# Performance work log

Hardware: AMD Instinct MI355X
Metric: run time of the kernel (lower is better)

The kernel has to match this reference:

```python
import jax, jax.numpy as jnp
import numpy as np

N, T, D, H = 32, 1024, 512, 512


def setup_inputs() -> dict:
    key = jax.random.key(0)
    k1, k2, k3, k4 = jax.random.split(key, 4)
    x = jax.random.normal(k1, (N, T, D), dtype=jnp.float32)
    h0 = jax.random.normal(k2, (N, H), dtype=jnp.float32)
    Wx = jax.random.normal(k3, (D, 4 * H), dtype=jnp.float32) / np.sqrt(D)
    Wh = jax.random.normal(k4, (H, 4 * H), dtype=jnp.float32) / np.sqrt(H)
    b = jnp.zeros((4 * H,), dtype=jnp.float32)
    return {"x": x, "h0": h0, "Wx": Wx, "Wh": Wh, "b": b}


def reference(x, h0, Wx, Wh, b):
    Hdim = h0.shape[1]
    # Precompute input projection for all timesteps: (N,T,4H)
    xW = jnp.einsum('ntd,dk->ntk', x, Wx) + b

    def step(carry, xw_t):
        h, c = carry
        a = xw_t + h @ Wh  # (N,4H)
        i = jax.nn.sigmoid(a[:, :Hdim])
        f = jax.nn.sigmoid(a[:, Hdim:2 * Hdim])
        o = jax.nn.sigmoid(a[:, 2 * Hdim:3 * Hdim])
        g = jnp.tanh(a[:, 3 * Hdim:])
        c_next = f * c + i * g
        h_next = o * jnp.tanh(c_next)
        return (h_next, c_next), h_next

    c0 = jnp.zeros_like(h0)
    xW_t = jnp.swapaxes(xW, 0, 1)  # (T,N,4H) for scan over time
    _, hs = jax.lax.scan(step, (h0, c0), xW_t)
    return jnp.swapaxes(hs, 0, 1)  # (N,T,H)
```

## Files before the change

kernel.cpp:

```cpp
#include <hip/hip_runtime.h>
#include <hip/hip_bf16.h>


#define NWG 32
#define LDW 520
#define SMEM_BYTES (2*64*LDW*2 + 4*32*16*4 + 512*4)

typedef __attribute__((ext_vector_type(8))) short s16x8;
typedef __attribute__((ext_vector_type(4))) float f32x4;
typedef __attribute__((ext_vector_type(4))) float f4v;

__device__ __forceinline__ float b2f(unsigned short u) {
  unsigned v = ((unsigned)u) << 16;
  return __builtin_bit_cast(float, v);
}
__device__ __forceinline__ unsigned short f2b(float f) {
  unsigned u = __builtin_bit_cast(unsigned, f);
  unsigned r = (u + 0x7fffu + ((u >> 16) & 1u)) >> 16;
  return (unsigned short)r;
}
__device__ __forceinline__ float sigmoidf_(float x) {
  return 1.f / (1.f + __expf(-x));
}
__device__ __forceinline__ float tanhf_(float x) {
  float ax = fabsf(x);
  float e = __expf(-2.f * ax);
  float th = (1.f - e) / (1.f + e);
  return copysignf(th, x);
}

__device__ __forceinline__ void store_short_mall(void* p, unsigned short v) {
  unsigned vv = v;
  asm volatile("global_store_short %0, %1, off sc0 sc1"
               :: "v"(p), "v"(vv) : "memory");
}
__device__ __forceinline__ void store_dword_mall(void* p, unsigned v) {
  asm volatile("global_store_dword %0, %1, off sc0 sc1"
               :: "v"(p), "v"(v) : "memory");
}
__device__ __forceinline__ unsigned load_dword_mall(const void* p) {
  unsigned r;
  asm volatile("global_load_dword %0, %1, off sc0 sc1\n\t"
               "s_waitcnt vmcnt(0)"
               : "=v"(r) : "v"(p) : "memory");
  return r;
}

__device__ __forceinline__ void split8(const float* p, s16x8& hi, s16x8& lo) {
  float tmp[8];
  *(f4v*)&tmp[0] = *(const f4v*)&p[0];
  *(f4v*)&tmp[4] = *(const f4v*)&p[4];
#pragma unroll
  for (int j = 0; j < 8; j++) {
    unsigned short h = f2b(tmp[j]);
    hi[j] = (short)h;
    lo[j] = (short)f2b(tmp[j] - b2f(h));
  }
}
__device__ __forceinline__ s16x8 cvt8(const float* p) {
  float tmp[8];
  *(f4v*)&tmp[0] = *(const f4v*)&p[0];
  *(f4v*)&tmp[4] = *(const f4v*)&p[4];
  s16x8 r;
#pragma unroll
  for (int j = 0; j < 8; j++) r[j] = (short)f2b(tmp[j]);
  return r;
}

__device__ __forceinline__ bool sniff_is_bf16(const unsigned short* wx) {
  int cnt = 0;
  for (int i = 0; i < 512; i++) {
    unsigned e = (wx[i] >> 7) & 0xFF;
    cnt += (e >= 0x60 && e <= 0x9F) ? 1 : 0;
  }
  return cnt >= 440;
}

template <bool F32>
__device__ __forceinline__ void lstm_body(
    const void* xv, const void* h0v, const void* Wxv, const void* Whv,
    const void* biasv, void* outv, unsigned* __restrict__ bar,
    unsigned char* smem) {
  unsigned short* WhS = (unsigned short*)smem;
  unsigned short* WxS = (unsigned short*)(smem + 64 * LDW * 2);
  float* gatebuf = (float*)(smem + 2 * 64 * LDW * 2);
  float* cbuf = (float*)(smem + 2 * 64 * LDW * 2 + 4 * 32 * 16 * 4);

  const unsigned short* xb = (const unsigned short*)xv;
  const float* xf = (const float*)xv;
  const unsigned short* h0b = (const unsigned short*)h0v;
  const float* h0f = (const float*)h0v;

  const int tid = threadIdx.x;
  const int g = tid >> 6;
  const int lane = tid & 63;
  const int lm = lane & 15;
  const int q = lane >> 4;
  const int w = blockIdx.x;

  for (int i = 0; i < 8; i++) {
    int id = tid + i * 256;
    int gate = id & 3;
    int k = id >> 2;
    size_t base = (size_t)k * 2048 + gate * 512 + w * 16;
    if (F32) {
      const float* px = (const float*)Wxv + base;
      const float* ph = (const float*)Whv + base;
#pragma unroll
      for (int seg = 0; seg < 4; seg++) {
        f4v vx = *(const f4v*)(px + seg * 4);
        f4v vh = *(const f4v*)(ph + seg * 4);
#pragma unroll
        for (int j = 0; j < 4; j++) {
          WxS[(gate * 16 + seg * 4 + j) * LDW + k] = f2b(vx[j]);
          WhS[(gate * 16 + seg * 4 + j) * LDW + k] = f2b(vh[j]);
        }
      }
    } else {
      const unsigned short* px = (const unsigned short*)Wxv + base;
      const unsigned short* ph = (const unsigned short*)Whv + base;
      s16x8 vx0 = *(const s16x8*)&px[0];
      s16x8 vx1 = *(const s16x8*)&px[8];
      s16x8 vh0 = *(const s16x8*)&ph[0];
      s16x8 vh1 = *(const s16x8*)&ph[8];
#pragma unroll
      for (int j = 0; j < 8; j++) {
        WxS[(gate * 16 + j) * LDW + k]     = (unsigned short)vx0[j];
        WxS[(gate * 16 + 8 + j) * LDW + k] = (unsigned short)vx1[j];
        WhS[(gate * 16 + j) * LDW + k]     = (unsigned short)vh0[j];
        WhS[(gate * 16 + 8 + j) * LDW + k] = (unsigned short)vh1[j];
      }
    }
  }
  cbuf[tid] = 0.f;
  cbuf[tid + 256] = 0.f;

  float bv[2][4];
  for (int pp = 0; pp < 2; pp++) {
    int p = tid + pp * 256;
    int j = p & 15;
    for (int qq = 0; qq < 4; qq++) {
      int idx = qq * 512 + w * 16 + j;
      bv[pp][qq] = F32 ? ((const float*)biasv)[idx]
                       : b2f(((const unsigned short*)biasv)[idx]);
    }
  }
  __syncthreads();

  for (int t = 0; t < 1024; t++) {
    f32x4 acc0 = {0.f, 0.f, 0.f, 0.f};
    f32x4 acc1 = {0.f, 0.f, 0.f, 0.f};

    if (F32) {
      for (int kc = 0; kc < 16; kc++) {
        int k = kc * 32 + q * 8;
        s16x8 bfrag = *(const s16x8*)&WxS[(g * 16 + lm) * LDW + k];
        s16x8 a0 = cvt8(&xf[(size_t)(lm * 1024 + t) * 512 + k]);
        s16x8 a1 = cvt8(&xf[(size_t)((16 + lm) * 1024 + t) * 512 + k]);
        acc0 = __builtin_amdgcn_mfma_f32_16x16x32_bf16(a0, bfrag, acc0, 0, 0, 0);
        acc1 = __builtin_amdgcn_mfma_f32_16x16x32_bf16(a1, bfrag, acc1, 0, 0, 0);
      }
    } else {
      for (int kc = 0; kc < 16; kc++) {
        int k = kc * 32 + q * 8;
        s16x8 bfrag = *(const s16x8*)&WxS[(g * 16 + lm) * LDW + k];
        s16x8 a0 = *(const s16x8*)&xb[(size_t)(lm * 1024 + t) * 512 + k];
        s16x8 a1 = *(const s16x8*)&xb[(size_t)((16 + lm) * 1024 + t) * 512 + k];
        acc0 = __builtin_amdgcn_mfma_f32_16x16x32_bf16(a0, bfrag, acc0, 0, 0, 0);
        acc1 = __builtin_amdgcn_mfma_f32_16x16x32_bf16(a1, bfrag, acc1, 0, 0, 0);
      }
    }

    if (t > 0) {
      if (tid < 64) {
        const unsigned target = (unsigned)t;
        const unsigned* fp = bar + (tid & 31);
        int guard = 0;
        for (;;) {
          unsigned v = load_dword_mall(fp);
          if (__all(v >= target)) break;
          if (++guard > (1 << 22)) break;
        }
      }
      __syncthreads();
      asm volatile("buffer_inv sc1" ::: "memory");
    }

    if (F32) {
      float* outf = (float*)outv;
      const float* hpf = (t == 0) ? h0f : outf + (size_t)(t - 1) * 512;
      const size_t hstride = (t == 0) ? 512 : (size_t)1024 * 512;
      for (int kc = 0; kc < 16; kc++) {
        int k = kc * 32 + q * 8;
        s16x8 bfrag = *(const s16x8*)&WhS[(g * 16 + lm) * LDW + k];
        s16x8 hi0, lo0, hi1, lo1;
        split8(&hpf[lm * hstride + k], hi0, lo0);
        split8(&hpf[(16 + lm) * hstride + k], hi1, lo1);
        acc0 = __builtin_amdgcn_mfma_f32_16x16x32_bf16(hi0, bfrag, acc0, 0, 0, 0);
        acc0 = __builtin_amdgcn_mfma_f32_16x16x32_bf16(lo0, bfrag, acc0, 0, 0, 0);
        acc1 = __builtin_amdgcn_mfma_f32_16x16x32_bf16(hi1, bfrag, acc1, 0, 0, 0);
        acc1 = __builtin_amdgcn_mfma_f32_16x16x32_bf16(lo1, bfrag, acc1, 0, 0, 0);
      }
    } else {
      unsigned short* outb = (unsigned short*)outv;
      const unsigned short* hpb = (t == 0) ? h0b : outb + (size_t)(t - 1) * 512;
      const size_t hstride = (t == 0) ? 512 : (size_t)1024 * 512;
      for (int kc = 0; kc < 16; kc++) {
        int k = kc * 32 + q * 8;
        s16x8 bfrag = *(const s16x8*)&WhS[(g * 16 + lm) * LDW + k];
        s16x8 a0 = *(const s16x8*)&hpb[lm * hstride + k];
        s16x8 a1 = *(const s16x8*)&hpb[(16 + lm) * hstride + k];
        acc0 = __builtin_amdgcn_mfma_f32_16x16x32_bf16(a0, bfrag, acc0, 0, 0, 0);
        acc1 = __builtin_amdgcn_mfma_f32_16x16x32_bf16(a1, bfrag, acc1, 0, 0, 0);
      }
    }

    for (int r = 0; r < 4; r++) {
      gatebuf[(g * 32 + q * 4 + r) * 16 + lm] = acc0[r];
      gatebuf[(g * 32 + 16 + q * 4 + r) * 16 + lm] = acc1[r];
    }
    __syncthreads();

    for (int pp = 0; pp < 2; pp++) {
      int p = tid + pp * 256;
      int n = p >> 4, j = p & 15;
      float ai = gatebuf[(0 * 32 + n) * 16 + j] + bv[pp][0];
      float af = gatebuf[(1 * 32 + n) * 16 + j] + bv[pp][1];
      float ao = gatebuf[(2 * 32 + n) * 16 + j] + bv[pp][2];
      float ag = gatebuf[(3 * 32 + n) * 16 + j] + bv[pp][3];
      float iG = sigmoidf_(ai);
      float fG = sigmoidf_(af);
      float oG = sigmoidf_(ao);
      float gG = tanhf_(ag);
      float c = fG * cbuf[p] + iG * gG;
      cbuf[p] = c;
      float h = oG * tanhf_(c);
      size_t oidx = (size_t)(n * 1024 + t) * 512 + w * 16 + j;
      if (F32) store_dword_mall((float*)outv + oidx,
                                __builtin_bit_cast(unsigned, h));
      else     store_short_mall((unsigned short*)outv + oidx, f2b(h));
    }
    asm volatile("s_waitcnt vmcnt(0)" ::: "memory");
    __syncthreads();

    if (t < 1023 && tid == 0) {
      unsigned done = (unsigned)(t + 1);
      store_dword_mall(bar + w, done);
    }
  }
}

__global__ __launch_bounds__(256) void lstm_kernel(
    const void* x, const void* h0, const void* Wx, const void* Wh,
    const void* bias, void* out, unsigned* bar) {
  extern __shared__ unsigned char smem[];
  if (sniff_is_bf16((const unsigned short*)Wx))
    lstm_body<false>(x, h0, Wx, Wh, bias, out, bar, smem);
  else
    lstm_body<true>(x, h0, Wx, Wh, bias, out, bar, smem);
}

extern "C" void kernel_launch(void* const* d_in, const int* in_sizes, int n_in,
                              void* d_out, int out_size, void* d_ws, size_t ws_size,
                              hipStream_t stream) {
  const void* x  = d_in[0];
  const void* h0 = d_in[1];
  const void* Wx = d_in[2];
  const void* Wh = d_in[3];
  const void* b  = d_in[4];
  void* out = d_out;
  unsigned* bar = (unsigned*)d_ws;

  hipMemsetAsync(bar, 0, 128, stream);

  hipFuncSetAttribute((const void*)lstm_kernel,
                      hipFuncAttributeMaxDynamicSharedMemorySize, SMEM_BYTES);

  void* args[] = {(void*)&x, (void*)&h0, (void*)&Wx, (void*)&Wh,
                  (void*)&b, (void*)&out, (void*)&bar};
  hipLaunchCooperativeKernel((const void*)lstm_kernel, dim3(NWG), dim3(256),
                             args, SMEM_BYTES, stream);
}
```

Baseline: 23.02 ms.

## Co-locate all worker blocks on one XCD and sync via L2 flags

The kernel now launches 256 workgroups. Each reads its XCC_ID and takes a rank within its XCD, and the first XCD to gather 32 blocks runs the LSTM using those ranks as block indices. The other blocks spin with FMA work and sleeps until a done flag is set. Because every worker shares one L2, the per-step flag stores and loads drop the sc1 system-scope bits, the cache invalidate becomes a plain buffer_inv, and h outputs use ordinary stores, all meant to cut cross-die barrier latency. The risks are weaker coherence if blocks are not actually co-located, the busy idle blocks drawing power, and a hang if no XCD ever gathers 32 resident blocks.

```diff
diff --git a/kernel.cpp b/kernel.cpp
--- a/kernel.cpp
+++ b/kernel.cpp
@@ -3,6 +3,7 @@
 
 
 #define NWG 32
+#define TOTAL_WG 256
 #define LDW 520
 #define SMEM_BYTES (2*64*LDW*2 + 4*32*16*4 + 512*4)
 
@@ -29,16 +30,22 @@
   return copysignf(th, x);
 }
 
-__device__ __forceinline__ void store_short_mall(void* p, unsigned short v) {
-  unsigned vv = v;
-  asm volatile("global_store_short %0, %1, off sc0 sc1"
-               :: "v"(p), "v"(vv) : "memory");
-}
-__device__ __forceinline__ void store_dword_mall(void* p, unsigned v) {
+__device__ __forceinline__ void store_flag_l2(unsigned* p, unsigned v) {
+  asm volatile("global_store_dword %0, %1, off sc0"
+               :: "v"(p), "v"(v) : "memory");
+}
+__device__ __forceinline__ unsigned load_flag_l2(const unsigned* p) {
+  unsigned r;
+  asm volatile("global_load_dword %0, %1, off sc0\n\t"
+               "s_waitcnt vmcnt(0)"
+               : "=v"(r) : "v"(p) : "memory");
+  return r;
+}
+__device__ __forceinline__ void store_dword_dev(unsigned* p, unsigned v) {
   asm volatile("global_store_dword %0, %1, off sc0 sc1"
                :: "v"(p), "v"(v) : "memory");
 }
-__device__ __forceinline__ unsigned load_dword_mall(const void* p) {
+__device__ __forceinline__ unsigned load_dword_dev(const unsigned* p) {
   unsigned r;
   asm volatile("global_load_dword %0, %1, off sc0 sc1\n\t"
                "s_waitcnt vmcnt(0)"
@@ -80,7 +87,7 @@
 __device__ __forceinline__ void lstm_body(
     const void* xv, const void* h0v, const void* Wxv, const void* Whv,
     const void* biasv, void* outv, unsigned* __restrict__ bar,
-    unsigned char* smem) {
+    unsigned char* smem, int w) {
   unsigned short* WhS = (unsigned short*)smem;
   unsigned short* WxS = (unsigned short*)(smem + 64 * LDW * 2);
   float* gatebuf = (float*)(smem + 2 * 64 * LDW * 2);
@@ -96,7 +103,6 @@
   const int lane = tid & 63;
   const int lm = lane & 15;
   const int q = lane >> 4;
-  const int w = blockIdx.x;
 
   for (int i = 0; i < 8; i++) {
     int id = tid + i * 256;
@@ -177,13 +183,13 @@
         const unsigned* fp = bar + (tid & 31);
         int guard = 0;
         for (;;) {
-          unsigned v = load_dword_mall(fp);
+          unsigned v = load_flag_l2(fp);
           if (__all(v >= target)) break;
           if (++guard > (1 << 22)) break;
         }
       }
       __syncthreads();
-      asm volatile("buffer_inv sc1" ::: "memory");
+      asm volatile("buffer_inv" ::: "memory");
     }
 
     if (F32) {
@@ -236,28 +242,63 @@
       cbuf[p] = c;
       float h = oG * tanhf_(c);
       size_t oidx = (size_t)(n * 1024 + t) * 512 + w * 16 + j;
-      if (F32) store_dword_mall((float*)outv + oidx,
-                                __builtin_bit_cast(unsigned, h));
-      else     store_short_mall((unsigned short*)outv + oidx, f2b(h));
+      if (F32) ((float*)outv)[oidx] = h;
+      else     ((unsigned short*)outv)[oidx] = f2b(h);
     }
     asm volatile("s_waitcnt vmcnt(0)" ::: "memory");
     __syncthreads();
 
     if (t < 1023 && tid == 0) {
-      unsigned done = (unsigned)(t + 1);
-      store_dword_mall(bar + w, done);
+      store_flag_l2(bar + w, (unsigned)(t + 1));
     }
   }
 }
 
 __global__ __launch_bounds__(256) void lstm_kernel(
     const void* x, const void* h0, const void* Wx, const void* Wh,
-    const void* bias, void* out, unsigned* bar) {
+    const void* bias, void* out, unsigned* ws) {
   extern __shared__ unsigned char smem[];
-  if (sniff_is_bf16((const unsigned short*)Wx))
-    lstm_body<false>(x, h0, Wx, Wh, bias, out, bar, smem);
-  else
-    lstm_body<true>(x, h0, Wx, Wh, bias, out, bar, smem);
+  __shared__ unsigned s_role[2];
+  unsigned* flags  = ws;
+  unsigned* cnt    = ws + 32;
+  unsigned* winner = ws + 48;
+  unsigned* done   = ws + 49;
+
+  if (threadIdx.x == 0) {
+    unsigned xcd;
+    asm volatile("s_getreg_b32 %0, hwreg(HW_REG_XCC_ID)" : "=s"(xcd));
+    xcd &= 0xFu;
+    unsigned rank = atomicAdd(&cnt[xcd], 1u);
+    if (rank == 31u) atomicCAS(winner, 0u, xcd + 1u);
+    unsigned wv; int guard = 0;
+    do {
+      wv = load_dword_dev(winner);
+    } while (wv == 0u && ++guard < (1 << 26));
+    s_role[0] = (wv == xcd + 1u && rank < 32u) ? 1u : 0u;
+    s_role[1] = rank;
+  }
+  __syncthreads();
+
+  if (s_role[0]) {
+    int w = (int)s_role[1];
+    if (sniff_is_bf16((const unsigned short*)Wx))
+      lstm_body<false>(x, h0, Wx, Wh, bias, out, flags, smem, w);
+    else
+      lstm_body<true>(x, h0, Wx, Wh, bias, out, flags, smem, w);
+    if (w == 0 && threadIdx.x == 0) store_dword_dev(done, 1u);
+  } else {
+    float a = 1.0f;
+    const float bm = 1.0000001f;
+    for (int o = 0; o < (1 << 22); ++o) {
+#pragma unroll
+      for (int i = 0; i < 64; i++) a = __builtin_fmaf(a, bm, 1e-7f);
+      __builtin_amdgcn_s_sleep(2);
+      if ((o & 63) == 0) {
+        if (load_dword_dev(done) != 0u) break;
+      }
+    }
+    asm volatile("" :: "v"(a));
+  }
 }
 
 extern "C" void kernel_launch(void* const* d_in, const int* in_sizes, int n_in,
@@ -269,15 +310,15 @@
   const void* Wh = d_in[3];
   const void* b  = d_in[4];
   void* out = d_out;
-  unsigned* bar = (unsigned*)d_ws;
-
-  hipMemsetAsync(bar, 0, 128, stream);
+  unsigned* ws = (unsigned*)d_ws;
+
+  hipMemsetAsync(ws, 0, 256, stream);
 
   hipFuncSetAttribute((const void*)lstm_kernel,
                       hipFuncAttributeMaxDynamicSharedMemorySize, SMEM_BYTES);
 
   void* args[] = {(void*)&x, (void*)&h0, (void*)&Wx, (void*)&Wh,
-                  (void*)&b, (void*)&out, (void*)&bar};
-  hipLaunchCooperativeKernel((const void*)lstm_kernel, dim3(NWG), dim3(256),
+                  (void*)&b, (void*)&out, (void*)&ws};
+  hipLaunchCooperativeKernel((const void*)lstm_kernel, dim3(TOTAL_WG), dim3(256),
                              args, SMEM_BYTES, stream);
 }
```

Result: slower. 25.44 ms (+10.5%).
